# Performance work log

Hardware: AMD Instinct MI355X
Metric: run time of the kernel (lower is better)

## Reference

```python
import jax, jax.numpy as jnp
import numpy as np

B, T, S = 2, 1024, 1024
D_Q, D_KV, D_OUT = 2048, 2048, 2048
N_Q, N_KV, H = 16, 4, 128
G = N_Q // N_KV  # GQA groups
MIN_TS, MAX_TS = 1.0, 10000.0
SDPA_SCALE = 1.0  # dia uses scale=1.0 in F.scaled_dot_product_attention


def setup_inputs() -> dict:
    key = jax.random.key(0)
    ks = jax.random.split(key, 6)
    Xq = jax.random.normal(ks[0], (B, T, D_Q), jnp.float32)
    Xkv = jax.random.normal(ks[1], (B, S, D_KV), jnp.float32)
    q_positions = jnp.broadcast_to(jnp.arange(T, dtype=jnp.int32), (B, T))
    kv_positions = jnp.broadcast_to(jnp.arange(S, dtype=jnp.int32), (B, S))
    Wq = jax.random.normal(ks[2], (D_Q, N_Q, H), jnp.float32) * (D_Q ** -0.5)
    Wk = jax.random.normal(ks[3], (D_KV, N_KV, H), jnp.float32) * (D_KV ** -0.5)
    Wv = jax.random.normal(ks[4], (D_KV, N_KV, H), jnp.float32) * (D_KV ** -0.5)
    Wo = jax.random.normal(ks[5], (N_Q, H, D_OUT), jnp.float32) * ((N_Q * H) ** -0.5)
    return {"Xq": Xq, "Xkv": Xkv, "q_positions": q_positions,
            "kv_positions": kv_positions, "Wq": Wq, "Wk": Wk, "Wv": Wv, "Wo": Wo}


def _apply_rope(x, positions):
    # x: (B, L, N, H); positions: (B, L) int
    half = H // 2
    fraction = 2.0 * jnp.arange(half, dtype=jnp.float32) / H
    timescale = MIN_TS * (MAX_TS / MIN_TS) ** fraction  # (half,)
    sinusoid = positions.astype(jnp.float32)[:, :, None, None] / timescale  # (B,L,1,half)
    sin, cos = jnp.sin(sinusoid), jnp.cos(sinusoid)
    x = x.astype(jnp.float32)
    x1, x2 = jnp.split(x, 2, axis=-1)
    return jnp.concatenate([x1 * cos - x2 * sin, x2 * cos + x1 * sin], axis=-1)


def reference(Xq, Xkv, q_positions, kv_positions, Wq, Wk, Wv, Wo):
    # QKV projections (DenseGeneral): (B,L,D) x (D,N,H) -> (B,L,N,H)
    q = jnp.einsum('btd,dnh->btnh', Xq, Wq)
    k = jnp.einsum('bsd,dnh->bsnh', Xkv, Wk)
    v = jnp.einsum('bsd,dnh->bsnh', Xkv, Wv)
    # RoPE on q and k
    q = _apply_rope(q, q_positions)
    k = _apply_rope(k, kv_positions)
    # GQA attention, scale = 1.0 (as in dia), no mask, non-causal
    q = q.transpose(0, 2, 1, 3).reshape(B, N_KV, G, T, H)  # (B,K,G,T,H)
    k = k.transpose(0, 2, 1, 3)                             # (B,K,S,H)
    v = v.transpose(0, 2, 1, 3)                             # (B,K,S,H)
    scores = jnp.einsum('bkgth,bksh->bkgts', q, k) * SDPA_SCALE
    probs = jax.nn.softmax(scores, axis=-1)
    attn = jnp.einsum('bkgts,bksh->bkgth', probs, v)        # (B,K,G,T,H)
    attn = attn.reshape(B, N_Q, T, H).transpose(0, 2, 1, 3)  # (B,T,N,H)
    # Output projection (DenseGeneral contracting (N,H))
    out = jnp.einsum('btnh,nho->bto', attn, Wo)
    return out
```

## Files before the change

### kernel.cpp

```cpp
#include <hip/hip_runtime.h>
#include <hip/hip_bf16.h>
#include <math.h>
#include <stdint.h>

#define B_SZ 2
#define T_SZ 1024
#define S_SZ 1024
#define NQ 16
#define NKV 4
#define HD 128
#define DQ 2048
#define DKV 2048
#define DOUT 2048

typedef _Float16 half8 __attribute__((ext_vector_type(8)));
typedef _Float16 half4 __attribute__((ext_vector_type(4)));
typedef float f32x4 __attribute__((ext_vector_type(4)));

__device__ __forceinline__ half8 load8_f16(const _Float16* p) {
    return *reinterpret_cast<const half8*>(p);
}

__device__ __forceinline__ void stage16(const _Float16* g, _Float16* l, int lane) {
#if __has_builtin(__builtin_amdgcn_global_load_lds)
    __builtin_amdgcn_global_load_lds(
        (const __attribute__((address_space(1))) uint32_t*)g,
        (__attribute__((address_space(3))) uint32_t*)l, 16, 0, 0);
#else
    *reinterpret_cast<half8*>(l + lane * 8) = *reinterpret_cast<const half8*>(g);
#endif
}

__device__ __forceinline__ void conv_blk(const float* __restrict__ in,
                                         _Float16* __restrict__ out, int vb) {
    size_t i = ((size_t)vb * 256 + threadIdx.x) * 8;
    float4 a = *reinterpret_cast<const float4*>(in + i);
    float4 b = *reinterpret_cast<const float4*>(in + i + 4);
    half8 r;
    r[0] = (_Float16)a.x; r[1] = (_Float16)a.y; r[2] = (_Float16)a.z; r[3] = (_Float16)a.w;
    r[4] = (_Float16)b.x; r[5] = (_Float16)b.y; r[6] = (_Float16)b.z; r[7] = (_Float16)b.w;
    *reinterpret_cast<half8*>(out + i) = r;
}

__device__ __forceinline__ void tr_blk(const float* __restrict__ in,
                                       _Float16* __restrict__ out,
                                       int R, int C, int bx, int by,
                                       _Float16 (*tile)[72]) {
    const int tx = threadIdx.x & 15, ty = threadIdx.x >> 4;
    const int r0 = by * 64, c0 = bx * 64;
    #pragma unroll
    for (int i = 0; i < 4; ++i) {
        int r = ty + i * 16;
        float4 v = *reinterpret_cast<const float4*>(&in[(size_t)(r0 + r) * C + c0 + tx * 4]);
        tile[r][tx * 4 + 0] = (_Float16)v.x;
        tile[r][tx * 4 + 1] = (_Float16)v.y;
        tile[r][tx * 4 + 2] = (_Float16)v.z;
        tile[r][tx * 4 + 3] = (_Float16)v.w;
    }
    __syncthreads();
    #pragma unroll
    for (int i = 0; i < 4; ++i) {
        int oc = ty + i * 16;
        half4 v;
        v[0] = tile[tx * 4 + 0][oc];
        v[1] = tile[tx * 4 + 1][oc];
        v[2] = tile[tx * 4 + 2][oc];
        v[3] = tile[tx * 4 + 3][oc];
        *reinterpret_cast<half4*>(&out[(size_t)(c0 + oc) * R + r0 + tx * 4]) = v;
    }
}

__device__ __forceinline__ void tr16_blk(const _Float16* __restrict__ in,
                                         _Float16* __restrict__ out,
                                         int Cin, int Cout, int r0, int c0,
                                         _Float16 (*tile)[72]) {
    const int tx = threadIdx.x & 15, ty = threadIdx.x >> 4;
    #pragma unroll
    for (int i = 0; i < 4; ++i) {
        int r = ty + i * 16;
        half4 v = *reinterpret_cast<const half4*>(&in[(size_t)(r0 + r) * Cin + c0 + tx * 4]);
        tile[r][tx * 4 + 0] = v[0];
        tile[r][tx * 4 + 1] = v[1];
        tile[r][tx * 4 + 2] = v[2];
        tile[r][tx * 4 + 3] = v[3];
    }
    __syncthreads();
    #pragma unroll
    for (int i = 0; i < 4; ++i) {
        int oc = ty + i * 16;
        half4 v;
        v[0] = tile[tx * 4 + 0][oc];
        v[1] = tile[tx * 4 + 1][oc];
        v[2] = tile[tx * 4 + 2][oc];
        v[3] = tile[tx * 4 + 3][oc];
        *reinterpret_cast<half4*>(&out[(size_t)(c0 + oc) * Cout + r0 + tx * 4]) = v;
    }
}

template <int NHEADS, int NSLOT, int RS>
__device__ __forceinline__ void rope_fast(_Float16* __restrict__ x,
                                          const int* __restrict__ pos, int vb) {
    const int t = vb * 256 + (int)threadIdx.x;
    const int hq = t & 15;
    const int ns = (t >> 4) % NSLOT;
    const int bl = (t >> 4) / NSLOT;
    const float p = (float)pos[bl];
    const float C = -0.2076205059304601f;
    float s[4], c[4];
    #pragma unroll
    for (int j = 0; j < 4; ++j) {
        float ang = p * exp2f((float)(hq * 4 + j) * C);
        s[j] = __sinf(ang);
        c[j] = __cosf(ang);
    }
    #pragma unroll
    for (int i = 0; i < NHEADS / NSLOT; ++i) {
        const int n = ns + i * NSLOT;
        size_t base = (size_t)bl * RS + (size_t)n * HD + hq * 4;
        half4 a  = *reinterpret_cast<half4*>(&x[base]);
        half4 b2 = *reinterpret_cast<half4*>(&x[base + 64]);
        half4 o1, o2;
        #pragma unroll
        for (int j = 0; j < 4; ++j) {
            float x1 = (float)a[j], x2 = (float)b2[j];
            o1[j] = (_Float16)(x1 * c[j] - x2 * s[j]);
            o2[j] = (_Float16)(x2 * c[j] + x1 * s[j]);
        }
        *reinterpret_cast<half4*>(&x[base])      = o1;
        *reinterpret_cast<half4*>(&x[base + 64]) = o2;
    }
}

__global__ __launch_bounds__(256) void prep1(const float* __restrict__ Xq, _Float16* __restrict__ Xq16,
                                             const float* __restrict__ Xkv, _Float16* __restrict__ Xkv16,
                                             const float* __restrict__ Wq, _Float16* __restrict__ WqT,
                                             const float* __restrict__ Wk, const float* __restrict__ Wv,
                                             _Float16* __restrict__ WkvT) {
    __shared__ _Float16 tile[64][72];
    int bx = blockIdx.x;
    if (bx < 2048) { conv_blk(Xq, Xq16, bx); return; }
    bx -= 2048;
    if (bx < 2048) { conv_blk(Xkv, Xkv16, bx); return; }
    bx -= 2048;
    if (bx < 1024) { tr_blk(Wq, WqT, 2048, 2048, bx & 31, bx >> 5, tile); return; }
    bx -= 1024;
    if (bx < 256) { tr_blk(Wk, WkvT, 2048, 512, bx & 7, bx >> 3, tile); return; }
    bx -= 256;
    tr_blk(Wv, WkvT + (size_t)512 * 2048, 2048, 512, bx & 7, bx >> 3, tile);
}

__global__ __launch_bounds__(256) void prep2(const float* __restrict__ Wo, _Float16* __restrict__ WoT,
                                             _Float16* __restrict__ Qh, const int* __restrict__ qpos,
                                             _Float16* __restrict__ KVh, const int* __restrict__ kpos,
                                             _Float16* __restrict__ VTh) {
    __shared__ _Float16 tile[64][72];
    int bx = blockIdx.x;
    if (bx < 1024) { tr_blk(Wo, WoT, 2048, 2048, bx & 31, bx >> 5, tile); return; }
    bx -= 1024;
    if (bx < 512) { rope_fast<NQ, 4, NQ * HD>(Qh, qpos, bx); return; }
    bx -= 512;
    if (bx < 256) { rope_fast<NKV, 2, 1024>(KVh, kpos, bx); return; }
    bx -= 256;
    {
        const int head = bx >> 5;
        const int t = bx & 31;
        const int sx = t & 15, hx = t >> 4;
        const int b = head >> 2, kn = head & 3;
        const _Float16* in = KVh + (size_t)(b * S_SZ) * 1024 + 512 + kn * HD;
        _Float16* out = VTh + (size_t)head * HD * S_SZ;
        tr16_blk(in, out, 1024, 1024, sx * 64, hx * 64, tile);
    }
}

template <int BM, int BN, typename TC>
__device__ __forceinline__ void gemm_tile(const _Float16* __restrict__ A,
                                          const _Float16* __restrict__ Bt,
                                          TC* __restrict__ C,
                                          int N, int K, int kbeg, int kend,
                                          int bm, int bn, _Float16* lds) {
    constexpr int ASEG = BM / 8, BSEG = BN / 8, TSEG = ASEG + BSEG, PSEG = TSEG / 4;
    constexpr int BUFSZ = TSEG * 512;
    const int tid = threadIdx.x, lane = tid & 63, w = tid >> 6;
    const int quad = lane >> 4, l16 = lane & 15;
    constexpr int WM = BM / 2, WN = BN / 2, MI = WM / 16, NI = WN / 16;
    const int wm = (w >> 1) * WM, wn = (w & 1) * WN;

    const int srl = lane >> 3;
    const int skb = (lane & 7) ^ srl;

    const _Float16* gp[PSEG];
    _Float16* lp[PSEG];
    #pragma unroll
    for (int p = 0; p < PSEG; ++p) {
        int s = w + p * 4;
        if (s < ASEG) {
            gp[p] = A + (size_t)(bm + s * 8 + srl) * K + kbeg + skb * 8;
        } else {
            gp[p] = Bt + (size_t)(bn + (s - ASEG) * 8 + srl) * K + kbeg + skb * 8;
        }
        lp[p] = lds + s * 512;
    }

    f32x4 acc[MI][NI];
    #pragma unroll
    for (int i = 0; i < MI; ++i)
        #pragma unroll
        for (int j = 0; j < NI; ++j)
            acc[i][j] = (f32x4){0.f, 0.f, 0.f, 0.f};

    const int nsteps = (kend - kbeg) >> 6;

    #pragma unroll
    for (int p = 0; p < PSEG; ++p)
        stage16(gp[p], lp[p], lane);
    __syncthreads();

    const int rxa = l16 & 7;
    int cur = 0;
    for (int it = 0; it < nsteps; ++it) {
        if (it + 1 < nsteps) {
            const int ko = (it + 1) * 64;
            const int nb = (cur ^ 1) * BUFSZ;
            #pragma unroll
            for (int p = 0; p < PSEG; ++p)
                stage16(gp[p] + ko, lp[p] + nb, lane);
        }
        const _Float16* lb = lds + cur * BUFSZ;
        #pragma unroll
        for (int h = 0; h < 2; ++h) {
            const int kb0 = h * 4 + quad;
            const int kswz = (kb0 ^ rxa) * 8;
            half8 af[MI], bf[NI];
            #pragma unroll
            for (int i = 0; i < MI; ++i) {
                const int r = wm + 16 * i + l16;
                af[i] = *reinterpret_cast<const half8*>(&lb[r * 64 + kswz]);
            }
            #pragma unroll
            for (int j = 0; j < NI; ++j) {
                const int r = wn + 16 * j + l16;
                bf[j] = *reinterpret_cast<const half8*>(&lb[BM * 64 + r * 64 + kswz]);
            }
            #pragma unroll
            for (int i = 0; i < MI; ++i)
                #pragma unroll
                for (int j = 0; j < NI; ++j)
                    acc[i][j] = __builtin_amdgcn_mfma_f32_16x16x32_f16(af[i], bf[j], acc[i][j], 0, 0, 0);
        }
        __syncthreads();
        cur ^= 1;
    }

    #pragma unroll
    for (int i = 0; i < MI; ++i)
        #pragma unroll
        for (int j = 0; j < NI; ++j)
            #pragma unroll
            for (int r = 0; r < 4; ++r) {
                size_t idx = (size_t)(bm + wm + 16 * i + quad * 4 + r) * N + bn + wn + 16 * j + l16;
                C[idx] = (TC)acc[i][j][r];
            }
}

__global__ __launch_bounds__(256) void proj_fused(const _Float16* __restrict__ Xq,
                                                  const _Float16* __restrict__ WqT,
                                                  _Float16* __restrict__ Qh,
                                                  const _Float16* __restrict__ Xkv,
                                                  const _Float16* __restrict__ WkvT,
                                                  _Float16* __restrict__ KVh) {
    __shared__ __align__(16) _Float16 lds[2 * (128 + 64) * 64];
    int bx = blockIdx.x;
    if (bx < 512) {
        gemm_tile<128, 64, _Float16>(Xq, WqT, Qh, 2048, 2048, 0, 2048,
                                     (bx & 15) * 128, (bx >> 4) * 64, lds);
    } else {
        bx -= 512;
        gemm_tile<128, 64, _Float16>(Xkv, WkvT, KVh, 1024, 2048, 0, 2048,
                                     (bx & 15) * 128, (bx >> 4) * 64, lds);
    }
}

__global__ __launch_bounds__(256) void gemm_out(const _Float16* __restrict__ A,
                                                const _Float16* __restrict__ Bt,
                                                float* __restrict__ C) {
    __shared__ __align__(16) _Float16 lds[2 * (128 + 64) * 64];
    const int bx = blockIdx.x;
    gemm_tile<128, 64, float>(A, Bt, C, 2048, 2048, 0, 2048,
                              (bx & 15) * 128, (bx >> 4) * 64, lds);
}

__global__ __launch_bounds__(256) void attn_kernel(const _Float16* __restrict__ Q,
                                                   const _Float16* __restrict__ KV,
                                                   const _Float16* __restrict__ VT,
                                                   _Float16* __restrict__ O) {
    constexpr int KBUF = 64 * 128;
    constexpr int VBUF = 128 * 64;
    constexpr int BUFSZ = KBUF + VBUF;
    __shared__ __align__(16) _Float16 lds[2 * BUFSZ];
    __shared__ __align__(16) _Float16 Ps[4][16][72];
    const int tid = threadIdx.x, lane = tid & 63, w = tid >> 6;
    const int quad = lane >> 4, l16 = lane & 15;
    const int hw = blockIdx.x;
    const int blk = (hw & 7) * 64 + (hw >> 3);
    const int t0 = (blk & 15) * 64;
    const int n  = (blk >> 4) & 15;
    const int b  = blk >> 8;
    const int kn = n >> 2;
    const _Float16* KVb  = KV + (size_t)b * S_SZ * 1024 + kn * HD;
    const _Float16* Vhead = VT + (size_t)(b * NKV + kn) * HD * S_SZ;

    const int krow_i = lane >> 4;
    const int kcp    = lane & 15;
    const int vrow_i = lane >> 3;
    const int vcp    = lane & 7;

    half8 qf[4];
    #pragma unroll
    for (int kh = 0; kh < 4; ++kh)
        qf[kh] = load8_f16(&Q[(((size_t)b * T_SZ + t0 + w * 16 + l16) * NQ + n) * HD + kh * 32 + quad * 8]);

    f32x4 o_acc[8];
    #pragma unroll
    for (int i = 0; i < 8; ++i) o_acc[i] = (f32x4){0.f, 0.f, 0.f, 0.f};
    float m_row[4] = {-1e30f, -1e30f, -1e30f, -1e30f};
    float l_part[4] = {0.f, 0.f, 0.f, 0.f};

    auto stage_tile = [&](int s0, int buf) {
        _Float16* kb = lds + buf * BUFSZ;
        _Float16* vb = kb + KBUF;
        #pragma unroll
        for (int j = 0; j < 4; ++j) {
            const int s = w + j * 4;
            const int row = 4 * s + krow_i;
            const int kc = kcp ^ (row & 7);
            stage16(KVb + (size_t)(s0 + row) * 1024 + kc * 8, kb + s * 512, lane);
        }
        #pragma unroll
        for (int j = 0; j < 4; ++j) {
            const int s = w + j * 4;
            const int row = 8 * s + vrow_i;
            const int vc = vcp ^ (row & 7);
            stage16(Vhead + (size_t)row * S_SZ + s0 + vc * 8, vb + s * 512, lane);
        }
    };

    stage_tile(0, 0);
    __syncthreads();

    const int rx = l16 & 7;
    int cur = 0;
    for (int t = 0; t < S_SZ / 64; ++t) {
        if (t + 1 < S_SZ / 64)
            stage_tile((t + 1) * 64, cur ^ 1);
        const _Float16* Kb = lds + cur * BUFSZ;
        const _Float16* Vb = Kb + KBUF;

        f32x4 sf[4];
        __builtin_amdgcn_s_setprio(1);
        #pragma unroll
        for (int i4 = 0; i4 < 4; ++i4) {
            const int srow = i4 * 16 + l16;
            f32x4 sa = (f32x4){0.f, 0.f, 0.f, 0.f};
            #pragma unroll
            for (int kh = 0; kh < 4; ++kh) {
                const int c = kh * 4 + quad;
                half8 bk = *reinterpret_cast<const half8*>(
                    &Kb[srow * 128 + ((c ^ rx) * 8)]);
                sa = __builtin_amdgcn_mfma_f32_16x16x32_f16(qf[kh], bk, sa, 0, 0, 0);
            }
            sf[i4] = sa;
        }
        __builtin_amdgcn_s_setprio(0);

        float mc[4];
        #pragma unroll
        for (int r = 0; r < 4; ++r) {
            float m0 = fmaxf(fmaxf(sf[0][r], sf[1][r]), fmaxf(sf[2][r], sf[3][r]));
            #pragma unroll
            for (int off = 1; off < 16; off <<= 1)
                m0 = fmaxf(m0, __shfl_xor(m0, off, 64));
            mc[r] = m0;
        }
        bool grow = (mc[0] > m_row[0] + 8.f) | (mc[1] > m_row[1] + 8.f) |
                    (mc[2] > m_row[2] + 8.f) | (mc[3] > m_row[3] + 8.f);
        if (__any(grow)) {
            #pragma unroll
            for (int r = 0; r < 4; ++r) {
                float mn = fmaxf(m_row[r], mc[r]);
                float alpha = __expf(m_row[r] - mn);
                m_row[r] = mn;
                l_part[r] *= alpha;
                #pragma unroll
                for (int ht = 0; ht < 8; ++ht)
                    o_acc[ht][r] *= alpha;
            }
        }
        #pragma unroll
        for (int r = 0; r < 4; ++r) {
            float p0 = __expf(sf[0][r] - m_row[r]);
            float p1 = __expf(sf[1][r] - m_row[r]);
            float p2 = __expf(sf[2][r] - m_row[r]);
            float p3 = __expf(sf[3][r] - m_row[r]);
            l_part[r] += (p0 + p1) + (p2 + p3);
            Ps[w][quad * 4 + r][l16]      = (_Float16)p0;
            Ps[w][quad * 4 + r][16 + l16] = (_Float16)p1;
            Ps[w][quad * 4 + r][32 + l16] = (_Float16)p2;
            Ps[w][quad * 4 + r][48 + l16] = (_Float16)p3;
        }
        __builtin_amdgcn_wave_barrier();
        half8 ap0 = *reinterpret_cast<const half8*>(&Ps[w][l16][quad * 8]);
        half8 ap1 = *reinterpret_cast<const half8*>(&Ps[w][l16][32 + quad * 8]);
        __builtin_amdgcn_wave_barrier();
        __builtin_amdgcn_s_setprio(1);
        #pragma unroll
        for (int ht = 0; ht < 8; ++ht) {
            const int vrow = ht * 16 + l16;
            half8 bv0 = *reinterpret_cast<const half8*>(
                &Vb[vrow * 64 + ((quad ^ rx) * 8)]);
            o_acc[ht] = __builtin_amdgcn_mfma_f32_16x16x32_f16(ap0, bv0, o_acc[ht], 0, 0, 0);
            half8 bv1 = *reinterpret_cast<const half8*>(
                &Vb[vrow * 64 + (((4 + quad) ^ rx) * 8)]);
            o_acc[ht] = __builtin_amdgcn_mfma_f32_16x16x32_f16(ap1, bv1, o_acc[ht], 0, 0, 0);
        }
        __builtin_amdgcn_s_setprio(0);

        __syncthreads();
        cur ^= 1;
    }

    float inv_l[4];
    #pragma unroll
    for (int r = 0; r < 4; ++r) {
        float l = l_part[r];
        #pragma unroll
        for (int off = 1; off < 16; off <<= 1)
            l += __shfl_xor(l, off, 64);
        inv_l[r] = 1.f / fmaxf(l, 1e-30f);
    }
    #pragma unroll
    for (int ht = 0; ht < 8; ++ht)
        #pragma unroll
        for (int r = 0; r < 4; ++r)
            O[(((size_t)b * T_SZ + t0 + w * 16 + quad * 4 + r) * NQ + n) * HD + ht * 16 + l16] =
                (_Float16)(o_acc[ht][r] * inv_l[r]);
}

extern "C" void kernel_launch(void* const* d_in, const int* in_sizes, int n_in,
                              void* d_out, int out_size, void* d_ws, size_t ws_size,
                              hipStream_t stream) {
    const float* Xq   = (const float*)d_in[0];
    const float* Xkv  = (const float*)d_in[1];
    const int*   qpos = (const int*)d_in[2];
    const int*   kpos = (const int*)d_in[3];
    const float* Wq   = (const float*)d_in[4];
    const float* Wk   = (const float*)d_in[5];
    const float* Wv   = (const float*)d_in[6];
    const float* Wo   = (const float*)d_in[7];
    float* out = (float*)d_out;

    const size_t SZ8 = 8388608;
    uint8_t* ws = (uint8_t*)d_ws;
    _Float16* Xq16  = (_Float16*)(ws);
    _Float16* Xkv16 = (_Float16*)(ws + SZ8);
    _Float16* WqT   = (_Float16*)(ws + 2 * SZ8);
    _Float16* WkvT  = (_Float16*)(ws + 3 * SZ8);
    _Float16* Qh    = (_Float16*)(ws + 3 * SZ8 + 4194304);
    _Float16* Ah  = Xq16;
    _Float16* WoT = Xkv16;
    _Float16* KVh = WqT;
    _Float16* VTh = WkvT;

    dim3 blk(256);
    prep1<<<5632, blk, 0, stream>>>(Xq, Xq16, Xkv, Xkv16, Wq, WqT, Wk, Wv, WkvT);
    proj_fused<<<768, blk, 0, stream>>>(Xq16, WqT, Qh, Xkv16, WkvT, KVh);
    prep2<<<2048, blk, 0, stream>>>(Wo, WoT, Qh, qpos, KVh, kpos, VTh);
    attn_kernel<<<512, blk, 0, stream>>>(Qh, KVh, VTh, Ah);
    gemm_out<<<512, blk, 0, stream>>>(Ah, WoT, out);
}
```

Measured before the change: 219.1 us.

## Software-pipeline attention: overlap previous tile's PV MFMA with current QK, DPP reductions

The attention KV tile shrinks from 64 to 32 rows, and the loop is restructured so the P·V MFMAs for tile t-1 issue right after the QK MFMAs for tile t. P goes into a double-buffered LDS array and V into a triple-buffered ring, which lets the softmax exp work overlap matrix math and removes the per-tile wave barriers. Row max and sum reductions switch from shfl_xor to DPP row-local moves. This adds a block-wide sync per half-size tile, which doubles the number of iterations and syncs, and the extra V buffer raises LDS use.

```diff
diff --git a/kernel.cpp b/kernel.cpp
--- a/kernel.cpp
+++ b/kernel.cpp
@@ -29,6 +29,22 @@
 #else
     *reinterpret_cast<half8*>(l + lane * 8) = *reinterpret_cast<const half8*>(g);
 #endif
+}
+
+#define DPPF(x, ctrl) __int_as_float(__builtin_amdgcn_mov_dpp(__float_as_int(x), ctrl, 0xF, 0xF, true))
+__device__ __forceinline__ float max16(float x) {
+    x = fmaxf(x, DPPF(x, 0xB1));
+    x = fmaxf(x, DPPF(x, 0x4E));
+    x = fmaxf(x, DPPF(x, 0x141));
+    x = fmaxf(x, DPPF(x, 0x140));
+    return x;
+}
+__device__ __forceinline__ float sum16(float x) {
+    x += DPPF(x, 0xB1);
+    x += DPPF(x, 0x4E);
+    x += DPPF(x, 0x141);
+    x += DPPF(x, 0x140);
+    return x;
 }
 
 __device__ __forceinline__ void conv_blk(const float* __restrict__ in,
@@ -293,11 +309,13 @@
                                                    const _Float16* __restrict__ KV,
                                                    const _Float16* __restrict__ VT,
                                                    _Float16* __restrict__ O) {
-    constexpr int KBUF = 64 * 128;
-    constexpr int VBUF = 128 * 64;
-    constexpr int BUFSZ = KBUF + VBUF;
-    __shared__ __align__(16) _Float16 lds[2 * BUFSZ];
-    __shared__ __align__(16) _Float16 Ps[4][16][72];
+    constexpr int KVB = 32;
+    constexpr int NT = S_SZ / KVB;
+    constexpr int KSLOT = KVB * 128;
+    constexpr int VSLOT = 128 * KVB;
+    __shared__ __align__(16) _Float16 Klds[2 * KSLOT];
+    __shared__ __align__(16) _Float16 Vlds[3 * VSLOT];
+    __shared__ __align__(16) _Float16 Ps[2][4][16][40];
     const int tid = threadIdx.x, lane = tid & 63, w = tid >> 6;
     const int quad = lane >> 4, l16 = lane & 15;
     const int hw = blockIdx.x;
@@ -306,13 +324,13 @@
     const int n  = (blk >> 4) & 15;
     const int b  = blk >> 8;
     const int kn = n >> 2;
-    const _Float16* KVb  = KV + (size_t)b * S_SZ * 1024 + kn * HD;
+    const _Float16* KVb   = KV + (size_t)b * S_SZ * 1024 + kn * HD;
     const _Float16* Vhead = VT + (size_t)(b * NKV + kn) * HD * S_SZ;
 
     const int krow_i = lane >> 4;
     const int kcp    = lane & 15;
-    const int vrow_i = lane >> 3;
-    const int vcp    = lane & 7;
+    const int vrow_i = lane >> 2;
+    const int vcp    = lane & 3;
 
     half8 qf[4];
     #pragma unroll
@@ -325,62 +343,70 @@
     float m_row[4] = {-1e30f, -1e30f, -1e30f, -1e30f};
     float l_part[4] = {0.f, 0.f, 0.f, 0.f};
 
-    auto stage_tile = [&](int s0, int buf) {
-        _Float16* kb = lds + buf * BUFSZ;
-        _Float16* vb = kb + KBUF;
-        #pragma unroll
-        for (int j = 0; j < 4; ++j) {
+    auto stage_K = [&](int s0, _Float16* kb) {
+        #pragma unroll
+        for (int j = 0; j < 2; ++j) {
             const int s = w + j * 4;
             const int row = 4 * s + krow_i;
             const int kc = kcp ^ (row & 7);
             stage16(KVb + (size_t)(s0 + row) * 1024 + kc * 8, kb + s * 512, lane);
         }
-        #pragma unroll
-        for (int j = 0; j < 4; ++j) {
+    };
+    auto stage_V = [&](int s0, _Float16* vb) {
+        #pragma unroll
+        for (int j = 0; j < 2; ++j) {
             const int s = w + j * 4;
-            const int row = 8 * s + vrow_i;
-            const int vc = vcp ^ (row & 7);
+            const int row = 16 * s + vrow_i;
+            const int vc = vcp ^ (row & 3);
             stage16(Vhead + (size_t)row * S_SZ + s0 + vc * 8, vb + s * 512, lane);
         }
     };
 
-    stage_tile(0, 0);
+    stage_K(0, Klds);
+    stage_V(0, Vlds);
     __syncthreads();
 
-    const int rx = l16 & 7;
-    int cur = 0;
-    for (int t = 0; t < S_SZ / 64; ++t) {
-        if (t + 1 < S_SZ / 64)
-            stage_tile((t + 1) * 64, cur ^ 1);
-        const _Float16* Kb = lds + cur * BUFSZ;
-        const _Float16* Vb = Kb + KBUF;
-
-        f32x4 sf[4];
+    int vprv = 2, vcur = 0, vnxt = 1;
+    for (int t = 0; t < NT; ++t) {
+        if (t + 1 < NT) {
+            stage_K((t + 1) * KVB, Klds + ((t + 1) & 1) * KSLOT);
+            stage_V((t + 1) * KVB, Vlds + vnxt * VSLOT);
+        }
+
+        const _Float16* Kb = Klds + (t & 1) * KSLOT;
+        f32x4 sf[2];
         __builtin_amdgcn_s_setprio(1);
         #pragma unroll
-        for (int i4 = 0; i4 < 4; ++i4) {
+        for (int i4 = 0; i4 < 2; ++i4) {
             const int srow = i4 * 16 + l16;
             f32x4 sa = (f32x4){0.f, 0.f, 0.f, 0.f};
             #pragma unroll
             for (int kh = 0; kh < 4; ++kh) {
                 const int c = kh * 4 + quad;
                 half8 bk = *reinterpret_cast<const half8*>(
-                    &Kb[srow * 128 + ((c ^ rx) * 8)]);
+                    &Kb[srow * 128 + ((c ^ (srow & 7)) * 8)]);
                 sa = __builtin_amdgcn_mfma_f32_16x16x32_f16(qf[kh], bk, sa, 0, 0, 0);
             }
             sf[i4] = sa;
         }
+
+        if (t > 0) {
+            half8 ap = *reinterpret_cast<const half8*>(&Ps[(t - 1) & 1][w][l16][quad * 8]);
+            const _Float16* Vb = Vlds + vprv * VSLOT;
+            #pragma unroll
+            for (int ht = 0; ht < 8; ++ht) {
+                const int vrow = ht * 16 + l16;
+                half8 bv = *reinterpret_cast<const half8*>(
+                    &Vb[vrow * 32 + ((quad ^ (vrow & 3)) * 8)]);
+                o_acc[ht] = __builtin_amdgcn_mfma_f32_16x16x32_f16(ap, bv, o_acc[ht], 0, 0, 0);
+            }
+        }
         __builtin_amdgcn_s_setprio(0);
 
         float mc[4];
         #pragma unroll
-        for (int r = 0; r < 4; ++r) {
-            float m0 = fmaxf(fmaxf(sf[0][r], sf[1][r]), fmaxf(sf[2][r], sf[3][r]));
-            #pragma unroll
-            for (int off = 1; off < 16; off <<= 1)
-                m0 = fmaxf(m0, __shfl_xor(m0, off, 64));
-            mc[r] = m0;
-        }
+        for (int r = 0; r < 4; ++r)
+            mc[r] = max16(fmaxf(sf[0][r], sf[1][r]));
         bool grow = (mc[0] > m_row[0] + 8.f) | (mc[1] > m_row[1] + 8.f) |
                     (mc[2] > m_row[2] + 8.f) | (mc[3] > m_row[3] + 8.f);
         if (__any(grow)) {
@@ -399,44 +425,33 @@
         for (int r = 0; r < 4; ++r) {
             float p0 = __expf(sf[0][r] - m_row[r]);
             float p1 = __expf(sf[1][r] - m_row[r]);
-            float p2 = __expf(sf[2][r] - m_row[r]);
-            float p3 = __expf(sf[3][r] - m_row[r]);
-            l_part[r] += (p0 + p1) + (p2 + p3);
-            Ps[w][quad * 4 + r][l16]      = (_Float16)p0;
-            Ps[w][quad * 4 + r][16 + l16] = (_Float16)p1;
-            Ps[w][quad * 4 + r][32 + l16] = (_Float16)p2;
-            Ps[w][quad * 4 + r][48 + l16] = (_Float16)p3;
-        }
-        __builtin_amdgcn_wave_barrier();
-        half8 ap0 = *reinterpret_cast<const half8*>(&Ps[w][l16][quad * 8]);
-        half8 ap1 = *reinterpret_cast<const half8*>(&Ps[w][l16][32 + quad * 8]);
-        __builtin_amdgcn_wave_barrier();
+            l_part[r] += p0 + p1;
+            Ps[t & 1][w][quad * 4 + r][l16]      = (_Float16)p0;
+            Ps[t & 1][w][quad * 4 + r][16 + l16] = (_Float16)p1;
+        }
+
+        __syncthreads();
+        int tmp = vprv; vprv = vcur; vcur = vnxt; vnxt = tmp;
+    }
+
+    {
+        half8 ap = *reinterpret_cast<const half8*>(&Ps[(NT - 1) & 1][w][l16][quad * 8]);
+        const _Float16* Vb = Vlds + vprv * VSLOT;
         __builtin_amdgcn_s_setprio(1);
         #pragma unroll
         for (int ht = 0; ht < 8; ++ht) {
             const int vrow = ht * 16 + l16;
-            half8 bv0 = *reinterpret_cast<const half8*>(
-                &Vb[vrow * 64 + ((quad ^ rx) * 8)]);
-            o_acc[ht] = __builtin_amdgcn_mfma_f32_16x16x32_f16(ap0, bv0, o_acc[ht], 0, 0, 0);
-            half8 bv1 = *reinterpret_cast<const half8*>(
-                &Vb[vrow * 64 + (((4 + quad) ^ rx) * 8)]);
-            o_acc[ht] = __builtin_amdgcn_mfma_f32_16x16x32_f16(ap1, bv1, o_acc[ht], 0, 0, 0);
+            half8 bv = *reinterpret_cast<const half8*>(
+                &Vb[vrow * 32 + ((quad ^ (vrow & 3)) * 8)]);
+            o_acc[ht] = __builtin_amdgcn_mfma_f32_16x16x32_f16(ap, bv, o_acc[ht], 0, 0, 0);
         }
         __builtin_amdgcn_s_setprio(0);
-
-        __syncthreads();
-        cur ^= 1;
     }
 
     float inv_l[4];
     #pragma unroll
-    for (int r = 0; r < 4; ++r) {
-        float l = l_part[r];
-        #pragma unroll
-        for (int off = 1; off < 16; off <<= 1)
-            l += __shfl_xor(l, off, 64);
-        inv_l[r] = 1.f / fmaxf(l, 1e-30f);
-    }
+    for (int r = 0; r < 4; ++r)
+        inv_l[r] = 1.f / fmaxf(sum16(l_part[r]), 1e-30f);
     #pragma unroll
     for (int ht = 0; ht < 8; ++ht)
         #pragma unroll
```

After: 234.5 us. +7.0%, slower.
